# Kernel optimization log

Measured on AMD Instinct MI355X. Metric: run time of the kernel, lower is better.

The kernel has to match this reference:

```python
import jax, jax.numpy as jnp
import numpy as np

LOG2_HASHMAP_SIZE = 19
HASHTABLE_SIZE = 2 ** LOG2_HASHMAP_SIZE
FEATURES_PER_LEVEL = 2
RES = 128
N_POINTS = 4194304

# Instant-NGP spatial hash primes (prime0 = 1)
_P1 = jnp.uint32(2654435761)
_P2 = jnp.uint32(805459861)


def _hash3(ix, iy, iz):
    # uint32 wrap-around multiply/xor matches torch int32 overflow bit pattern;
    # modulus is a power of two, so uint32 mod == floored int32 mod low bits.
    h = ix.astype(jnp.uint32) ^ (iy.astype(jnp.uint32) * _P1) ^ (iz.astype(jnp.uint32) * _P2)
    return (h % jnp.uint32(HASHTABLE_SIZE)).astype(jnp.int32)


def setup_inputs() -> dict:
    key = jax.random.key(0)
    kx, kt = jax.random.split(key)
    x = jax.random.uniform(kx, (N_POINTS, 3), dtype=jnp.float32)
    # hashtable = rand*2-1, scaled by hashmap_scale (=1)
    hashtable = jax.random.uniform(kt, (HASHTABLE_SIZE, FEATURES_PER_LEVEL), dtype=jnp.float32) * 2.0 - 1.0
    return {"x": x, "hashtable": hashtable}


def reference(x, hashtable):
    xr = x.reshape(-1, 3)
    x_scaled = xr * RES
    xf = jnp.floor(x_scaled).astype(jnp.int32)   # [N,3]
    xc = jnp.ceil(x_scaled).astype(jnp.int32)    # [N,3]

    fx, fy, fz = xf[:, 0], xf[:, 1], xf[:, 2]
    cx, cy, cz = xc[:, 0], xc[:, 1], xc[:, 2]

    # 8 corner hashes, ordering matches (h0..h7) = (000,100,010,001,110,101,011,111)
    h000 = _hash3(fx, fy, fz)
    h100 = _hash3(cx, fy, fz)
    h010 = _hash3(fx, cy, fz)
    h001 = _hash3(fx, fy, cz)
    h110 = _hash3(cx, cy, fz)
    h101 = _hash3(cx, fy, cz)
    h011 = _hash3(fx, cy, cz)
    h111 = _hash3(cx, cy, cz)

    idx = jnp.stack([h000, h100, h010, h001, h110, h101, h011, h111], axis=0)  # [8,N]
    v = hashtable[idx]  # [8, N, F] scattered gather
    v000, v100, v010, v001, v110, v101, v011, v111 = v

    d = x_scaled - xf.astype(x_scaled.dtype)  # [N,3] fractional offsets
    dx = d[:, 0:1]
    dy = d[:, 1:2]
    dz = d[:, 2:3]

    c00 = v000 * (1 - dx) + v100 * dx
    c01 = v001 * (1 - dx) + v101 * dx
    c10 = v010 * (1 - dx) + v110 * dx
    c11 = v011 * (1 - dx) + v111 * dx
    c0 = c00 * (1 - dy) + c10 * dy
    c1 = c01 * (1 - dy) + c11 * dy
    out = c0 * (1 - dz) + c1 * dz  # [N, F]

    return out.reshape(x.shape[:-1] + (FEATURES_PER_LEVEL,))
```

## Files before the change

### kernel.cpp

```cpp
#include <hip/hip_runtime.h>
#include <stdint.h>

#define LOG2_HASHMAP_SIZE 19
#define HASHTABLE_SIZE (1u << LOG2_HASHMAP_SIZE)
#define HASHTABLE_MASK (HASHTABLE_SIZE - 1u)
#define RES_F 128.0f

typedef float f32x2 __attribute__((ext_vector_type(2)));
typedef float f32x4 __attribute__((ext_vector_type(4)));
typedef uint32_t u32x4 __attribute__((ext_vector_type(4)));

__device__ __forceinline__ f32x4 nt_load4(const f32x4* p) {
    return __builtin_nontemporal_load(p);
}
__device__ __forceinline__ void nt_store4(f32x4* p, f32x4 v) {
    __builtin_nontemporal_store(v, p);
}

__device__ __forceinline__ float bf16w_lo(uint32_t w) {
    return __uint_as_float(w << 16);
}
__device__ __forceinline__ float bf16w_hi(uint32_t w) {
    return __uint_as_float(w & 0xFFFF0000u);
}

__device__ __forceinline__ uint32_t pack_bf16x2(float a, float b) {
    uint32_t ua = __float_as_uint(a);
    uint32_t ub = __float_as_uint(b);
    ua = ua + 0x7FFFu + ((ua >> 16) & 1u);
    ub = ub + 0x7FFFu + ((ub >> 16) & 1u);
    return (ua >> 16) | (ub & 0xFFFF0000u);
}

__global__ __launch_bounds__(256) void convert_table_kernel(
    const f32x4* __restrict__ table4,
    u32x4* __restrict__ ws4)
{
    int i = blockIdx.x * blockDim.x + threadIdx.x;
    f32x4 e01 = table4[2 * i + 0];
    f32x4 e23 = table4[2 * i + 1];
    u32x4 o;
    o.x = pack_bf16x2(e01.x, e01.y);
    o.y = pack_bf16x2(e01.z, e01.w);
    o.z = pack_bf16x2(e23.x, e23.y);
    o.w = pack_bf16x2(e23.z, e23.w);
    ws4[i] = o;
}

__global__ __launch_bounds__(256) void featurefield_bf16_kernel(
    const f32x4* __restrict__ x4,
    const uint32_t* __restrict__ tb,
    f32x4* __restrict__ out4,
    int n_quads)
{
    int t = blockIdx.x * blockDim.x + threadIdx.x;
    if (t >= n_quads) return;

    const u32x4* tb4 = (const u32x4*)tb;

    f32x4 a = nt_load4(&x4[3 * t + 0]);
    f32x4 b = nt_load4(&x4[3 * t + 1]);
    f32x4 c = nt_load4(&x4[3 * t + 2]);

    float px[4] = {a.x, a.w, b.z, c.y};
    float py[4] = {a.y, b.x, b.w, c.z};
    float pz[4] = {a.z, b.y, c.x, c.w};

    uint32_t i0[4][4];
    uint32_t mm[4];
    float dxs[4], dys[4], dzs[4];

    #pragma unroll
    for (int k = 0; k < 4; ++k) {
        float xs = px[k] * RES_F;
        float ys = py[k] * RES_F;
        float zs = pz[k] * RES_F;
        float fxf = floorf(xs), fyf = floorf(ys), fzf = floorf(zs);
        int fx = (int)fxf, fy = (int)fyf, fz = (int)fzf;
        int cx = (int)ceilf(xs), cy = (int)ceilf(ys), cz = (int)ceilf(zs);
        dxs[k] = xs - fxf;
        dys[k] = ys - fyf;
        dzs[k] = zs - fzf;

        uint32_t ufx = (uint32_t)fx;
        mm[k] = ufx ^ (uint32_t)cx;
        uint32_t fyp = (uint32_t)fy * 2654435761u;
        uint32_t cyp = (uint32_t)cy * 2654435761u;
        uint32_t fzp = (uint32_t)fz * 805459861u;
        uint32_t czp = (uint32_t)cz * 805459861u;

        i0[k][0] = (ufx ^ fyp ^ fzp) & HASHTABLE_MASK;
        i0[k][1] = (ufx ^ cyp ^ fzp) & HASHTABLE_MASK;
        i0[k][2] = (ufx ^ fyp ^ czp) & HASHTABLE_MASK;
        i0[k][3] = (ufx ^ cyp ^ czp) & HASHTABLE_MASK;
    }

    u32x4 q[4][4];
    #pragma unroll
    for (int k = 0; k < 4; ++k) {
        #pragma unroll
        for (int j = 0; j < 4; ++j) {
            q[k][j] = tb4[i0[k][j] >> 2];
        }
    }

    uint32_t w0[4][4], w1[4][4];
    #pragma unroll
    for (int k = 0; k < 4; ++k) {
        #pragma unroll
        for (int j = 0; j < 4; ++j) {
            uint32_t e0 = i0[k][j] & 3u;
            uint32_t e1 = (i0[k][j] ^ mm[k]) & 3u;
            uint32_t qq[4] = {q[k][j].x, q[k][j].y, q[k][j].z, q[k][j].w};
            w0[k][j] = qq[e0];
            w1[k][j] = qq[e1];
        }
        if (mm[k] > 3u) {
            #pragma unroll
            for (int j = 0; j < 4; ++j) {
                w1[k][j] = tb[i0[k][j] ^ mm[k]];
            }
        }
    }

    f32x2 res[4];
    #pragma unroll
    for (int k = 0; k < 4; ++k) {
        float dx = dxs[k], dy = dys[k], dz = dzs[k];
        float wx = 1.0f - dx, wy = 1.0f - dy, wz = 1.0f - dz;

        float c00x = bf16w_lo(w0[k][0]) * wx + bf16w_lo(w1[k][0]) * dx;
        float c00y = bf16w_hi(w0[k][0]) * wx + bf16w_hi(w1[k][0]) * dx;
        float c10x = bf16w_lo(w0[k][1]) * wx + bf16w_lo(w1[k][1]) * dx;
        float c10y = bf16w_hi(w0[k][1]) * wx + bf16w_hi(w1[k][1]) * dx;
        float c01x = bf16w_lo(w0[k][2]) * wx + bf16w_lo(w1[k][2]) * dx;
        float c01y = bf16w_hi(w0[k][2]) * wx + bf16w_hi(w1[k][2]) * dx;
        float c11x = bf16w_lo(w0[k][3]) * wx + bf16w_lo(w1[k][3]) * dx;
        float c11y = bf16w_hi(w0[k][3]) * wx + bf16w_hi(w1[k][3]) * dx;

        float c0x = c00x * wy + c10x * dy;
        float c0y = c00y * wy + c10y * dy;
        float c1x = c01x * wy + c11x * dy;
        float c1y = c01y * wy + c11y * dy;

        res[k].x = c0x * wz + c1x * dz;
        res[k].y = c0y * wz + c1y * dz;
    }

    f32x4 o0 = {res[0].x, res[0].y, res[1].x, res[1].y};
    f32x4 o1 = {res[2].x, res[2].y, res[3].x, res[3].y};
    nt_store4(&out4[2 * t + 0], o0);
    nt_store4(&out4[2 * t + 1], o1);
}

__global__ __launch_bounds__(256) void featurefield_fp32_kernel(
    const f32x4* __restrict__ x4,
    const float2* __restrict__ table,
    f32x4* __restrict__ out4,
    int n_quads)
{
    int t = blockIdx.x * blockDim.x + threadIdx.x;
    if (t >= n_quads) return;

    f32x4 a = nt_load4(&x4[3 * t + 0]);
    f32x4 b = nt_load4(&x4[3 * t + 1]);
    f32x4 c = nt_load4(&x4[3 * t + 2]);

    float px[4] = {a.x, a.w, b.z, c.y};
    float py[4] = {a.y, b.x, b.w, c.z};
    float pz[4] = {a.z, b.y, c.x, c.w};

    uint32_t h[4][8];
    float dxs[4], dys[4], dzs[4];

    #pragma unroll
    for (int k = 0; k < 4; ++k) {
        float xs = px[k] * RES_F, ys = py[k] * RES_F, zs = pz[k] * RES_F;
        float fxf = floorf(xs), fyf = floorf(ys), fzf = floorf(zs);
        int fx = (int)fxf, fy = (int)fyf, fz = (int)fzf;
        int cx = (int)ceilf(xs), cy = (int)ceilf(ys), cz = (int)ceilf(zs);
        dxs[k] = xs - fxf; dys[k] = ys - fyf; dzs[k] = zs - fzf;
        uint32_t ufx = (uint32_t)fx, ucx = (uint32_t)cx;
        uint32_t fyp = (uint32_t)fy * 2654435761u, cyp = (uint32_t)cy * 2654435761u;
        uint32_t fzp = (uint32_t)fz * 805459861u, czp = (uint32_t)cz * 805459861u;
        h[k][0] = (ufx ^ fyp ^ fzp) & HASHTABLE_MASK;
        h[k][1] = (ucx ^ fyp ^ fzp) & HASHTABLE_MASK;
        h[k][2] = (ufx ^ cyp ^ fzp) & HASHTABLE_MASK;
        h[k][3] = (ufx ^ fyp ^ czp) & HASHTABLE_MASK;
        h[k][4] = (ucx ^ cyp ^ fzp) & HASHTABLE_MASK;
        h[k][5] = (ucx ^ fyp ^ czp) & HASHTABLE_MASK;
        h[k][6] = (ufx ^ cyp ^ czp) & HASHTABLE_MASK;
        h[k][7] = (ucx ^ cyp ^ czp) & HASHTABLE_MASK;
    }

    float2 v[4][8];
    #pragma unroll
    for (int k = 0; k < 4; ++k)
        #pragma unroll
        for (int j = 0; j < 8; ++j)
            v[k][j] = table[h[k][j]];

    f32x2 res[4];
    #pragma unroll
    for (int k = 0; k < 4; ++k) {
        float dx = dxs[k], dy = dys[k], dz = dzs[k];
        float wx = 1.0f - dx, wy = 1.0f - dy, wz = 1.0f - dz;
        float c00x = v[k][0].x * wx + v[k][1].x * dx;
        float c00y = v[k][0].y * wx + v[k][1].y * dx;
        float c01x = v[k][3].x * wx + v[k][5].x * dx;
        float c01y = v[k][3].y * wx + v[k][5].y * dx;
        float c10x = v[k][2].x * wx + v[k][4].x * dx;
        float c10y = v[k][2].y * wx + v[k][4].y * dx;
        float c11x = v[k][6].x * wx + v[k][7].x * dx;
        float c11y = v[k][6].y * wx + v[k][7].y * dx;
        float c0x = c00x * wy + c10x * dy;
        float c0y = c00y * wy + c10y * dy;
        float c1x = c01x * wy + c11x * dy;
        float c1y = c01y * wy + c11y * dy;
        res[k].x = c0x * wz + c1x * dz;
        res[k].y = c0y * wz + c1y * dz;
    }

    f32x4 o0 = {res[0].x, res[0].y, res[1].x, res[1].y};
    f32x4 o1 = {res[2].x, res[2].y, res[3].x, res[3].y};
    nt_store4(&out4[2 * t + 0], o0);
    nt_store4(&out4[2 * t + 1], o1);
}

extern "C" void kernel_launch(void* const* d_in, const int* in_sizes, int n_in,
                              void* d_out, int out_size, void* d_ws, size_t ws_size,
                              hipStream_t stream) {
    const f32x4* x4 = (const f32x4*)d_in[0];
    f32x4* out4 = (f32x4*)d_out;

    int n_points = in_sizes[0] / 3;
    int n_quads = n_points / 4;
    int block = 256;
    int grid = (n_quads + block - 1) / block;

    size_t need = (size_t)HASHTABLE_SIZE * 4u;
    if (ws_size >= need) {
        const f32x4* table4 = (const f32x4*)d_in[1];
        u32x4* ws4 = (u32x4*)d_ws;
        int conv_threads = HASHTABLE_SIZE / 4;
        convert_table_kernel<<<conv_threads / 256, 256, 0, stream>>>(table4, ws4);
        featurefield_bf16_kernel<<<grid, block, 0, stream>>>(
            x4, (const uint32_t*)d_ws, out4, n_quads);
    } else {
        const float2* table = (const float2*)d_in[1];
        featurefield_fp32_kernel<<<grid, block, 0, stream>>>(x4, table, out4, n_quads);
    }
}
```

Measured before the change: 179.0 us.

## Process two points per thread with buffer loads and higher occupancy bound

```diff
diff --git a/kernel.cpp b/kernel.cpp
--- a/kernel.cpp
+++ b/kernel.cpp
@@ -9,8 +9,27 @@
 typedef float f32x2 __attribute__((ext_vector_type(2)));
 typedef float f32x4 __attribute__((ext_vector_type(4)));
 typedef uint32_t u32x4 __attribute__((ext_vector_type(4)));
-
-__device__ __forceinline__ f32x4 nt_load4(const f32x4* p) {
+typedef int i32x4 __attribute__((ext_vector_type(4)));
+
+__device__ u32x4 llvm_amdgcn_raw_buffer_load_v4u32(i32x4 rsrc, int voffset,
+                                                   int soffset, int aux)
+    __asm("llvm.amdgcn.raw.buffer.load.v4i32");
+__device__ uint32_t llvm_amdgcn_raw_buffer_load_u32(i32x4 rsrc, int voffset,
+                                                    int soffset, int aux)
+    __asm("llvm.amdgcn.raw.buffer.load.i32");
+
+__device__ __forceinline__ i32x4 make_srd(const void* p, uint32_t bytes) {
+    union { const void* p; uint32_t u[2]; } a;
+    a.p = p;
+    i32x4 r;
+    r.x = (int)a.u[0];
+    r.y = (int)(a.u[1] & 0xFFFFu);
+    r.z = (int)bytes;
+    r.w = 0x00020000;
+    return r;
+}
+
+__device__ __forceinline__ f32x2 nt_load2(const f32x2* p) {
     return __builtin_nontemporal_load(p);
 }
 __device__ __forceinline__ void nt_store4(f32x4* p, f32x4 v) {
@@ -22,6 +41,12 @@
 }
 __device__ __forceinline__ float bf16w_hi(uint32_t w) {
     return __uint_as_float(w & 0xFFFF0000u);
+}
+
+__device__ __forceinline__ uint32_t sel4(u32x4 q, uint32_t e) {
+    uint32_t lo = (e & 1u) ? q.y : q.x;
+    uint32_t hi = (e & 1u) ? q.w : q.z;
+    return (e & 2u) ? hi : lo;
 }
 
 __device__ __forceinline__ uint32_t pack_bf16x2(float a, float b) {
@@ -47,31 +72,31 @@
     ws4[i] = o;
 }
 
-__global__ __launch_bounds__(256) void featurefield_bf16_kernel(
-    const f32x4* __restrict__ x4,
+__global__ __launch_bounds__(256, 8) void featurefield_bf16_kernel(
+    const f32x2* __restrict__ x2,
     const uint32_t* __restrict__ tb,
     f32x4* __restrict__ out4,
-    int n_quads)
+    int n_pairs)
 {
     int t = blockIdx.x * blockDim.x + threadIdx.x;
-    if (t >= n_quads) return;
-
-    const u32x4* tb4 = (const u32x4*)tb;
-
-    f32x4 a = nt_load4(&x4[3 * t + 0]);
-    f32x4 b = nt_load4(&x4[3 * t + 1]);
-    f32x4 c = nt_load4(&x4[3 * t + 2]);
-
-    float px[4] = {a.x, a.w, b.z, c.y};
-    float py[4] = {a.y, b.x, b.w, c.z};
-    float pz[4] = {a.z, b.y, c.x, c.w};
-
-    uint32_t i0[4][4];
-    uint32_t mm[4];
-    float dxs[4], dys[4], dzs[4];
-
-    #pragma unroll
-    for (int k = 0; k < 4; ++k) {
+    if (t >= n_pairs) return;
+
+    i32x4 srd = make_srd(tb, HASHTABLE_SIZE * 4u);
+
+    f32x2 A = nt_load2(&x2[3 * t + 0]);
+    f32x2 B = nt_load2(&x2[3 * t + 1]);
+    f32x2 C = nt_load2(&x2[3 * t + 2]);
+
+    float px[2] = {A.x, B.y};
+    float py[2] = {A.y, C.x};
+    float pz[2] = {B.x, C.y};
+
+    uint32_t i0[2][4];
+    uint32_t mm[2];
+    float dxs[2], dys[2], dzs[2];
+
+    #pragma unroll
+    for (int k = 0; k < 2; ++k) {
         float xs = px[k] * RES_F;
         float ys = py[k] * RES_F;
         float zs = pz[k] * RES_F;
@@ -95,37 +120,37 @@
         i0[k][3] = (ufx ^ cyp ^ czp) & HASHTABLE_MASK;
     }
 
-    u32x4 q[4][4];
-    #pragma unroll
-    for (int k = 0; k < 4; ++k) {
+    u32x4 q[2][4];
+    #pragma unroll
+    for (int k = 0; k < 2; ++k) {
         #pragma unroll
         for (int j = 0; j < 4; ++j) {
-            q[k][j] = tb4[i0[k][j] >> 2];
+            q[k][j] = llvm_amdgcn_raw_buffer_load_v4u32(
+                srd, (int)((i0[k][j] << 2) & ~15u), 0, 0);
         }
     }
 
-    uint32_t w0[4][4], w1[4][4];
-    #pragma unroll
-    for (int k = 0; k < 4; ++k) {
+    uint32_t w0[2][4], w1[2][4];
+    #pragma unroll
+    for (int k = 0; k < 2; ++k) {
         #pragma unroll
         for (int j = 0; j < 4; ++j) {
             uint32_t e0 = i0[k][j] & 3u;
-            uint32_t e1 = (i0[k][j] ^ mm[k]) & 3u;
-            uint32_t qq[4] = {q[k][j].x, q[k][j].y, q[k][j].z, q[k][j].w};
-            w0[k][j] = qq[e0];
-            w1[k][j] = qq[e1];
+            w0[k][j] = sel4(q[k][j], e0);
+            w1[k][j] = sel4(q[k][j], e0 ^ (mm[k] & 3u));
         }
         if (mm[k] > 3u) {
             #pragma unroll
             for (int j = 0; j < 4; ++j) {
-                w1[k][j] = tb[i0[k][j] ^ mm[k]];
+                w1[k][j] = llvm_amdgcn_raw_buffer_load_u32(
+                    srd, (int)((i0[k][j] ^ mm[k]) << 2), 0, 0);
             }
         }
     }
 
-    f32x2 res[4];
-    #pragma unroll
-    for (int k = 0; k < 4; ++k) {
+    f32x2 res[2];
+    #pragma unroll
+    for (int k = 0; k < 2; ++k) {
         float dx = dxs[k], dy = dys[k], dz = dzs[k];
         float wx = 1.0f - dx, wy = 1.0f - dy, wz = 1.0f - dz;
 
@@ -147,96 +172,75 @@
         res[k].y = c0y * wz + c1y * dz;
     }
 
-    f32x4 o0 = {res[0].x, res[0].y, res[1].x, res[1].y};
-    f32x4 o1 = {res[2].x, res[2].y, res[3].x, res[3].y};
-    nt_store4(&out4[2 * t + 0], o0);
-    nt_store4(&out4[2 * t + 1], o1);
+    f32x4 o = {res[0].x, res[0].y, res[1].x, res[1].y};
+    nt_store4(&out4[t], o);
 }
 
 __global__ __launch_bounds__(256) void featurefield_fp32_kernel(
-    const f32x4* __restrict__ x4,
+    const f32x2* __restrict__ x2,
     const float2* __restrict__ table,
     f32x4* __restrict__ out4,
-    int n_quads)
+    int n_pairs)
 {
     int t = blockIdx.x * blockDim.x + threadIdx.x;
-    if (t >= n_quads) return;
-
-    f32x4 a = nt_load4(&x4[3 * t + 0]);
-    f32x4 b = nt_load4(&x4[3 * t + 1]);
-    f32x4 c = nt_load4(&x4[3 * t + 2]);
-
-    float px[4] = {a.x, a.w, b.z, c.y};
-    float py[4] = {a.y, b.x, b.w, c.z};
-    float pz[4] = {a.z, b.y, c.x, c.w};
-
-    uint32_t h[4][8];
-    float dxs[4], dys[4], dzs[4];
-
-    #pragma unroll
-    for (int k = 0; k < 4; ++k) {
+    if (t >= n_pairs) return;
+
+    f32x2 A = nt_load2(&x2[3 * t + 0]);
+    f32x2 B = nt_load2(&x2[3 * t + 1]);
+    f32x2 C = nt_load2(&x2[3 * t + 2]);
+
+    float px[2] = {A.x, B.y};
+    float py[2] = {A.y, C.x};
+    float pz[2] = {B.x, C.y};
+
+    f32x2 res[2];
+    #pragma unroll
+    for (int k = 0; k < 2; ++k) {
         float xs = px[k] * RES_F, ys = py[k] * RES_F, zs = pz[k] * RES_F;
         float fxf = floorf(xs), fyf = floorf(ys), fzf = floorf(zs);
         int fx = (int)fxf, fy = (int)fyf, fz = (int)fzf;
         int cx = (int)ceilf(xs), cy = (int)ceilf(ys), cz = (int)ceilf(zs);
-        dxs[k] = xs - fxf; dys[k] = ys - fyf; dzs[k] = zs - fzf;
+        float dx = xs - fxf, dy = ys - fyf, dz = zs - fzf;
         uint32_t ufx = (uint32_t)fx, ucx = (uint32_t)cx;
         uint32_t fyp = (uint32_t)fy * 2654435761u, cyp = (uint32_t)cy * 2654435761u;
         uint32_t fzp = (uint32_t)fz * 805459861u, czp = (uint32_t)cz * 805459861u;
-        h[k][0] = (ufx ^ fyp ^ fzp) & HASHTABLE_MASK;
-        h[k][1] = (ucx ^ fyp ^ fzp) & HASHTABLE_MASK;
-        h[k][2] = (ufx ^ cyp ^ fzp) & HASHTABLE_MASK;
-        h[k][3] = (ufx ^ fyp ^ czp) & HASHTABLE_MASK;
-        h[k][4] = (ucx ^ cyp ^ fzp) & HASHTABLE_MASK;
-        h[k][5] = (ucx ^ fyp ^ czp) & HASHTABLE_MASK;
-        h[k][6] = (ufx ^ cyp ^ czp) & HASHTABLE_MASK;
-        h[k][7] = (ucx ^ cyp ^ czp) & HASHTABLE_MASK;
-    }
-
-    float2 v[4][8];
-    #pragma unroll
-    for (int k = 0; k < 4; ++k)
-        #pragma unroll
-        for (int j = 0; j < 8; ++j)
-            v[k][j] = table[h[k][j]];
-
-    f32x2 res[4];
-    #pragma unroll
-    for (int k = 0; k < 4; ++k) {
-        float dx = dxs[k], dy = dys[k], dz = dzs[k];
+        uint32_t h0 = (ufx ^ fyp ^ fzp) & HASHTABLE_MASK;
+        uint32_t h1 = (ucx ^ fyp ^ fzp) & HASHTABLE_MASK;
+        uint32_t h2 = (ufx ^ cyp ^ fzp) & HASHTABLE_MASK;
+        uint32_t h3 = (ufx ^ fyp ^ czp) & HASHTABLE_MASK;
+        uint32_t h4 = (ucx ^ cyp ^ fzp) & HASHTABLE_MASK;
+        uint32_t h5 = (ucx ^ fyp ^ czp) & HASHTABLE_MASK;
+        uint32_t h6 = (ufx ^ cyp ^ czp) & HASHTABLE_MASK;
+        uint32_t h7 = (ucx ^ cyp ^ czp) & HASHTABLE_MASK;
+
+        float2 v0 = table[h0], v1 = table[h1], v2 = table[h2], v3 = table[h3];
+        float2 v4 = table[h4], v5 = table[h5], v6 = table[h6], v7 = table[h7];
+
         float wx = 1.0f - dx, wy = 1.0f - dy, wz = 1.0f - dz;
-        float c00x = v[k][0].x * wx + v[k][1].x * dx;
-        float c00y = v[k][0].y * wx + v[k][1].y * dx;
-        float c01x = v[k][3].x * wx + v[k][5].x * dx;
-        float c01y = v[k][3].y * wx + v[k][5].y * dx;
-        float c10x = v[k][2].x * wx + v[k][4].x * dx;
-        float c10y = v[k][2].y * wx + v[k][4].y * dx;
-        float c11x = v[k][6].x * wx + v[k][7].x * dx;
-        float c11y = v[k][6].y * wx + v[k][7].y * dx;
-        float c0x = c00x * wy + c10x * dy;
-        float c0y = c00y * wy + c10y * dy;
-        float c1x = c01x * wy + c11x * dy;
-        float c1y = c01y * wy + c11y * dy;
+        float c00x = v0.x * wx + v1.x * dx, c00y = v0.y * wx + v1.y * dx;
+        float c01x = v3.x * wx + v5.x * dx, c01y = v3.y * wx + v5.y * dx;
+        float c10x = v2.x * wx + v4.x * dx, c10y = v2.y * wx + v4.y * dx;
+        float c11x = v6.x * wx + v7.x * dx, c11y = v6.y * wx + v7.y * dx;
+        float c0x = c00x * wy + c10x * dy, c0y = c00y * wy + c10y * dy;
+        float c1x = c01x * wy + c11x * dy, c1y = c01y * wy + c11y * dy;
         res[k].x = c0x * wz + c1x * dz;
         res[k].y = c0y * wz + c1y * dz;
     }
 
-    f32x4 o0 = {res[0].x, res[0].y, res[1].x, res[1].y};
-    f32x4 o1 = {res[2].x, res[2].y, res[3].x, res[3].y};
-    nt_store4(&out4[2 * t + 0], o0);
-    nt_store4(&out4[2 * t + 1], o1);
+    f32x4 o = {res[0].x, res[0].y, res[1].x, res[1].y};
+    nt_store4(&out4[t], o);
 }
 
 extern "C" void kernel_launch(void* const* d_in, const int* in_sizes, int n_in,
                               void* d_out, int out_size, void* d_ws, size_t ws_size,
                               hipStream_t stream) {
-    const f32x4* x4 = (const f32x4*)d_in[0];
+    const f32x2* x2 = (const f32x2*)d_in[0];
     f32x4* out4 = (f32x4*)d_out;
 
     int n_points = in_sizes[0] / 3;
-    int n_quads = n_points / 4;
+    int n_pairs = n_points / 2;
     int block = 256;
-    int grid = (n_quads + block - 1) / block;
+    int grid = (n_pairs + block - 1) / block;
 
     size_t need = (size_t)HASHTABLE_SIZE * 4u;
     if (ws_size >= need) {
@@ -245,9 +249,9 @@
         int conv_threads = HASHTABLE_SIZE / 4;
         convert_table_kernel<<<conv_threads / 256, 256, 0, stream>>>(table4, ws4);
         featurefield_bf16_kernel<<<grid, block, 0, stream>>>(
-            x4, (const uint32_t*)d_ws, out4, n_quads);
+            x2, (const uint32_t*)d_ws, out4, n_pairs);
     } else {
         const float2* table = (const float2*)d_in[1];
-        featurefield_fp32_kernel<<<grid, block, 0, stream>>>(x4, table, out4, n_quads);
-    }
-}
+        featurefield_fp32_kernel<<<grid, block, 0, stream>>>(x2, table, out4, n_pairs);
+    }
+}
```

New measurement: 178.4 us. No clear change (-0.4%).
